# Performance work log

Hardware: AMD Instinct MI355X
Metric: run time of the kernel (lower is better)

The kernel has to match this reference:

```python
import jax, jax.numpy as jnp
import numpy as np

NUM_EXPERTS = 8
NUM_SLOTS = 4

def setup_inputs() -> dict:
    key = jax.random.key(0)
    k1, k2 = jax.random.split(key)
    B, S, D = 8, 4096, 1024
    x = jax.random.normal(k1, (B, S, D), dtype=jnp.float32)
    W_phi = jax.random.normal(k2, (D, NUM_EXPERTS * NUM_SLOTS), dtype=jnp.float32) * (1.0 / np.sqrt(D))
    b_phi = jnp.zeros((NUM_EXPERTS * NUM_SLOTS,), dtype=jnp.float32)
    return {"x": x, "W_phi": W_phi, "b_phi": b_phi}

def reference(x, W_phi, b_phi):
    B, S, D = x.shape
    E, P = NUM_EXPERTS, NUM_SLOTS
    # phi logits: (B, S, E, P)
    phi_logits = (jnp.einsum('bsd,dk->bsk', x, W_phi) + b_phi).reshape(B, S, E, P)
    # softmax over seq axis (dispatch weights)
    phi_weights = jax.nn.softmax(phi_logits, axis=1)
    # soft slots: weighted sum of tokens per (expert, slot) -> (B, E, P, D)
    # (faithful to expand_dims*multiply*sum-over-seq in the original, fused as einsum)
    soft_slots = jnp.einsum('bsep,bsd->bepd', phi_weights, x)
    expert_inputs = soft_slots.reshape(B, E, P * D)
    expert_weights = jnp.full((B, S, E), 1.0 / E, dtype=x.dtype)
    expert_indices = jnp.broadcast_to(jnp.arange(E, dtype=jnp.int32)[None, None, :], (B, S, E))
    raw_gate_probs = jax.nn.softmax(phi_logits, axis=-1)
    return (expert_weights, expert_indices, phi_weights, soft_slots, expert_inputs, phi_logits, raw_gate_probs)
```

## Files before the change

### kernel.cpp

```cpp
#include <hip/hip_runtime.h>
#include <hip/hip_bf16.h>

#define BB 8
#define SS 4096
#define DD 1024
#define KK 32
#define EE 8
#define PP 4

#define O0 0L
#define O1 262144L
#define O2 524288L
#define O3 1572864L
#define O4 1835008L
#define O5 2097152L
#define O6 3145728L

#define WA 0L
#define WB 8192L
#define WC 16384L
#define WPKH (WC + 2097152L)
#define WPKL (WPKH + 16384L)
#define WEND (WPKL + 16384L)

typedef __attribute__((ext_vector_type(8))) short short8v;
typedef __attribute__((ext_vector_type(4))) float f32x4;

__device__ __forceinline__ unsigned short f2bf(float f) {
    unsigned u = __builtin_bit_cast(unsigned, f);
    unsigned r = (u + 0x7FFFu + ((u >> 16) & 1u)) >> 16;
    return (unsigned short)r;
}
__device__ __forceinline__ float bf2f(unsigned short h) {
    return __builtin_bit_cast(float, (unsigned)h << 16);
}

__global__ __launch_bounds__(256) void k_wprep(const float* __restrict__ Wp,
    unsigned short* __restrict__ wh, unsigned short* __restrict__ wl)
{
    const int t  = blockIdx.x * 256 + threadIdx.x;
    const int l  = t & 63;
    const int tt = (t >> 6) & 1;
    const int ks = t >> 7;
    const int col = tt * 16 + (l & 15);
    const int dbase = ks * 32 + (l >> 4) * 8;
    const long obase = ((long)(ks * 2 + tt) * 64 + l) * 8;
#pragma unroll
    for (int j = 0; j < 8; ++j) {
        const float w = Wp[(long)(dbase + j) * KK + col];
        const unsigned short h = f2bf(w);
        const float lo = w - bf2f(h);
        wh[obase + j] = h;
        wl[obase + j] = f2bf(lo);
    }
}

__global__ __launch_bounds__(256) void k_logits_mfma(const float* __restrict__ x,
    const unsigned short* __restrict__ wh, const unsigned short* __restrict__ wl,
    float* __restrict__ wsP)
{
    const int tid  = threadIdx.x;
    const int wv   = tid >> 6;
    const int lane = tid & 63;
    const int blk  = blockIdx.x;
    const int tile = blk >> 1, half = blk & 1;
    const long tokw = (long)tile * 64 + wv * 16;
    const int mrow = lane & 15;
    const int kg   = lane >> 4;

    const float* xr = x + (tokw + mrow) * DD + half * 512 + kg * 8;
    const uint4* bh = reinterpret_cast<const uint4*>(wh) + (long)half * 16 * 2 * 64 + lane;
    const uint4* bl = reinterpret_cast<const uint4*>(wl) + (long)half * 16 * 2 * 64 + lane;

    f32x4 acc0 = {0.f, 0.f, 0.f, 0.f};
    f32x4 acc1 = {0.f, 0.f, 0.f, 0.f};

#pragma unroll 4
    for (int s = 0; s < 16; ++s) {
        const float4 u0 = *reinterpret_cast<const float4*>(xr + s * 32);
        const float4 u1 = *reinterpret_cast<const float4*>(xr + s * 32 + 4);
        const short8v b0h = __builtin_bit_cast(short8v, bh[(long)(s * 2    ) * 64]);
        const short8v b1h = __builtin_bit_cast(short8v, bh[(long)(s * 2 + 1) * 64]);
        const short8v b0l = __builtin_bit_cast(short8v, bl[(long)(s * 2    ) * 64]);
        const short8v b1l = __builtin_bit_cast(short8v, bl[(long)(s * 2 + 1) * 64]);

        const float xf[8] = {u0.x, u0.y, u0.z, u0.w, u1.x, u1.y, u1.z, u1.w};
        short8v ah, al;
#pragma unroll
        for (int j = 0; j < 8; ++j) {
            const unsigned u = __builtin_bit_cast(unsigned, xf[j]);
            ah[j] = (short)(u >> 16);
            const float hi = __builtin_bit_cast(float, u & 0xFFFF0000u);
            const float lo = xf[j] - hi;
            al[j] = (short)(__builtin_bit_cast(unsigned, lo) >> 16);
        }
        acc0 = __builtin_amdgcn_mfma_f32_16x16x32_bf16(ah, b0h, acc0, 0, 0, 0);
        acc1 = __builtin_amdgcn_mfma_f32_16x16x32_bf16(ah, b1h, acc1, 0, 0, 0);
        acc0 = __builtin_amdgcn_mfma_f32_16x16x32_bf16(al, b0h, acc0, 0, 0, 0);
        acc1 = __builtin_amdgcn_mfma_f32_16x16x32_bf16(al, b1h, acc1, 0, 0, 0);
        acc0 = __builtin_amdgcn_mfma_f32_16x16x32_bf16(ah, b0l, acc0, 0, 0, 0);
        acc1 = __builtin_amdgcn_mfma_f32_16x16x32_bf16(ah, b1l, acc1, 0, 0, 0);
    }

#pragma unroll
    for (int r = 0; r < 4; ++r) {
        const long tok = tokw + kg * 4 + r;
        float* o = wsP + ((long)half * 32768 + tok) * KK + mrow;
        o[0]  = acc0[r];
        o[16] = acc1[r];
    }
}

__global__ __launch_bounds__(256) void k_comb2(const float* __restrict__ wsP,
    const float* __restrict__ bp, float* __restrict__ out, float* __restrict__ ws)
{
    const int blk = blockIdx.x;
    const int tid = threadIdx.x;
    const int wv  = __builtin_amdgcn_readfirstlane(tid >> 6);
    const long g  = (long)blk * 256 + tid;
    float acc[KK];
#pragma unroll
    for (int k = 0; k < KK; ++k) acc[k] = bp[k];
#pragma unroll
    for (int h = 0; h < 2; ++h) {
        const float4* p = reinterpret_cast<const float4*>(wsP + ((long)h * 32768 + g) * KK);
#pragma unroll
        for (int m = 0; m < 8; ++m) {
            const float4 v = p[m];
            acc[4*m]   += v.x;
            acc[4*m+1] += v.y;
            acc[4*m+2] += v.z;
            acc[4*m+3] += v.w;
        }
    }
    float4* pl = reinterpret_cast<float4*>(out + O5 + g * KK);
#pragma unroll
    for (int m = 0; m < 8; ++m)
        pl[m] = make_float4(acc[4*m], acc[4*m+1], acc[4*m+2], acc[4*m+3]);
    float rg[KK];
#pragma unroll
    for (int e = 0; e < EE; ++e) {
        const float mx = fmaxf(fmaxf(acc[4*e], acc[4*e+1]), fmaxf(acc[4*e+2], acc[4*e+3]));
        float s = 0.f;
#pragma unroll
        for (int p = 0; p < PP; ++p) { rg[4*e+p] = __expf(acc[4*e+p] - mx); s += rg[4*e+p]; }
        const float ri = 1.f / s;
#pragma unroll
        for (int p = 0; p < PP; ++p) rg[4*e+p] *= ri;
    }
    float4* prg = reinterpret_cast<float4*>(out + O6 + g * KK);
#pragma unroll
    for (int m = 0; m < 8; ++m)
        prg[m] = make_float4(rg[4*m], rg[4*m+1], rg[4*m+2], rg[4*m+3]);
    float4* pew = reinterpret_cast<float4*>(out + O0 + g * EE);
    pew[0] = make_float4(0.125f, 0.125f, 0.125f, 0.125f);
    pew[1] = make_float4(0.125f, 0.125f, 0.125f, 0.125f);
    float4* pei = reinterpret_cast<float4*>(out + O1 + g * EE);
    pei[0] = make_float4(0.f, 1.f, 2.f, 3.f);
    pei[1] = make_float4(4.f, 5.f, 6.f, 7.f);

    float m[KK];
#pragma unroll
    for (int k = 0; k < KK; ++k) m[k] = acc[k];
    for (int off = 1; off < 64; off <<= 1) {
#pragma unroll
        for (int k = 0; k < KK; ++k) m[k] = fmaxf(m[k], __shfl_xor(m[k], off));
    }
    __shared__ float lm[4][KK];
    __shared__ float lsum[4][KK];
    if ((tid & 63) == 0) {
#pragma unroll
        for (int k = 0; k < KK; ++k) lm[wv][k] = m[k];
    }
    __syncthreads();
#pragma unroll
    for (int k = 0; k < KK; ++k)
        m[k] = fmaxf(fmaxf(lm[0][k], lm[1][k]), fmaxf(lm[2][k], lm[3][k]));
    float sv[KK];
#pragma unroll
    for (int k = 0; k < KK; ++k) sv[k] = __expf(acc[k] - m[k]);
    for (int off = 1; off < 64; off <<= 1) {
#pragma unroll
        for (int k = 0; k < KK; ++k) sv[k] += __shfl_xor(sv[k], off);
    }
    if ((tid & 63) == 0) {
#pragma unroll
        for (int k = 0; k < KK; ++k) lsum[wv][k] = sv[k];
    }
    __syncthreads();
    if (tid == 0) {
#pragma unroll
        for (int k = 0; k < KK; ++k) {
            ws[WA + (long)blk * 64 + k]      = m[k];
            ws[WA + (long)blk * 64 + 32 + k] = lsum[0][k] + lsum[1][k] + lsum[2][k] + lsum[3][k];
        }
    }
}

__global__ __launch_bounds__(256) void k_logits4(const float* __restrict__ x,
    const float* __restrict__ Wp, const float* __restrict__ bp,
    float* __restrict__ out)
{
    __shared__ float xl[2][64][68];
    __shared__ float wl[2][64][32];
    const int tid  = threadIdx.x;
    const int wv   = __builtin_amdgcn_readfirstlane(tid >> 6);
    const int lane = tid & 63;
    const long tok0 = (long)blockIdx.x * 64;
    const long g   = tok0 + lane;
    const int sr = tid >> 2;
    const int sco = (tid & 3) * 4;
    float acc[8];
#pragma unroll
    for (int j = 0; j < 8; ++j) acc[j] = 0.f;
    float4 xr[4], wr[2];
#pragma unroll
    for (int j = 0; j < 4; ++j)
        xr[j] = *reinterpret_cast<const float4*>(x + (tok0 + sr) * DD + sco + j * 16);
#pragma unroll
    for (int j = 0; j < 2; ++j)
        wr[j] = *reinterpret_cast<const float4*>(Wp + tid * 8 + j * 4);
#pragma unroll
    for (int j = 0; j < 4; ++j)
        *reinterpret_cast<float4*>(&xl[0][sr][sco + j * 16]) = xr[j];
#pragma unroll
    for (int j = 0; j < 2; ++j)
        *reinterpret_cast<float4*>(&wl[0][0][0] + tid * 8 + j * 4) = wr[j];
    __syncthreads();
    for (int c = 0; c < 16; ++c) {
        const int cb = c & 1;
        if (c < 15) {
            const long dg = (long)(c + 1) * 64;
#pragma unroll
            for (int j = 0; j < 4; ++j)
                xr[j] = *reinterpret_cast<const float4*>(
                    x + (tok0 + sr) * DD + dg + sco + j * 16);
#pragma unroll
            for (int j = 0; j < 2; ++j)
                wr[j] = *reinterpret_cast<const float4*>(Wp + dg * KK + tid * 8 + j * 4);
        }
        const float* xb = &xl[cb][lane][0];
        const float* wb = &wl[cb][0][0] + wv * 8;
#pragma unroll 4
        for (int dq = 0; dq < 16; ++dq) {
            const float4 xv = *reinterpret_cast<const float4*>(xb + dq * 4);
#pragma unroll
            for (int dd = 0; dd < 4; ++dd) {
                const float xs = (dd == 0) ? xv.x : (dd == 1) ? xv.y
                               : (dd == 2) ? xv.z : xv.w;
                const float4 w0 = *reinterpret_cast<const float4*>(wb + (dq * 4 + dd) * 32);
                const float4 w1 = *reinterpret_cast<const float4*>(wb + (dq * 4 + dd) * 32 + 4);
                acc[0] = fmaf(xs, w0.x, acc[0]);
                acc[1] = fmaf(xs, w0.y, acc[1]);
                acc[2] = fmaf(xs, w0.z, acc[2]);
                acc[3] = fmaf(xs, w0.w, acc[3]);
                acc[4] = fmaf(xs, w1.x, acc[4]);
                acc[5] = fmaf(xs, w1.y, acc[5]);
                acc[6] = fmaf(xs, w1.z, acc[6]);
                acc[7] = fmaf(xs, w1.w, acc[7]);
            }
        }
        if (c < 15) {
#pragma unroll
            for (int j = 0; j < 4; ++j)
                *reinterpret_cast<float4*>(&xl[cb ^ 1][sr][sco + j * 16]) = xr[j];
#pragma unroll
            for (int j = 0; j < 2; ++j)
                *reinterpret_cast<float4*>(&wl[cb ^ 1][0][0] + tid * 8 + j * 4) = wr[j];
        }
        __syncthreads();
    }
#pragma unroll
    for (int j = 0; j < 8; ++j) acc[j] += bp[wv * 8 + j];
    float* o5 = out + O5 + g * KK + wv * 8;
    *reinterpret_cast<float4*>(o5)     = make_float4(acc[0], acc[1], acc[2], acc[3]);
    *reinterpret_cast<float4*>(o5 + 4) = make_float4(acc[4], acc[5], acc[6], acc[7]);
    float rg[8];
#pragma unroll
    for (int e = 0; e < 2; ++e) {
        const float* aa = &acc[e * 4];
        const float m = fmaxf(fmaxf(aa[0], aa[1]), fmaxf(aa[2], aa[3]));
        float s = 0.f;
#pragma unroll
        for (int p = 0; p < PP; ++p) { rg[e*4+p] = __expf(aa[p] - m); s += rg[e*4+p]; }
        const float ri = 1.f / s;
#pragma unroll
        for (int p = 0; p < PP; ++p) rg[e*4+p] *= ri;
    }
    float* o6 = out + O6 + g * KK + wv * 8;
    *reinterpret_cast<float4*>(o6)     = make_float4(rg[0], rg[1], rg[2], rg[3]);
    *reinterpret_cast<float4*>(o6 + 4) = make_float4(rg[4], rg[5], rg[6], rg[7]);
    if (wv == 0) {
        float4* p = reinterpret_cast<float4*>(out + O0 + g * EE);
        p[0] = make_float4(0.125f, 0.125f, 0.125f, 0.125f);
        p[1] = make_float4(0.125f, 0.125f, 0.125f, 0.125f);
    } else if (wv == 1) {
        float4* p = reinterpret_cast<float4*>(out + O1 + g * EE);
        p[0] = make_float4(0.f, 1.f, 2.f, 3.f);
        p[1] = make_float4(4.f, 5.f, 6.f, 7.f);
    }
}

__global__ __launch_bounds__(256) void k_smpart(const float* __restrict__ out,
                                                float* __restrict__ ws)
{
    const int blk = blockIdx.x;
    const int tid = threadIdx.x;
    const int wv  = __builtin_amdgcn_readfirstlane(tid >> 6);
    const int b = blk >> 4, sc = blk & 15;
    const long s  = (long)sc * 256 + tid;
    const float* row = out + O5 + ((long)b * SS + s) * KK;
    float v[KK];
    const float4* r4 = reinterpret_cast<const float4*>(row);
#pragma unroll
    for (int q = 0; q < 8; ++q) {
        const float4 t = r4[q];
        v[4*q] = t.x; v[4*q+1] = t.y; v[4*q+2] = t.z; v[4*q+3] = t.w;
    }
    float m[KK];
#pragma unroll
    for (int k = 0; k < KK; ++k) m[k] = v[k];
    for (int off = 1; off < 64; off <<= 1) {
#pragma unroll
        for (int k = 0; k < KK; ++k) m[k] = fmaxf(m[k], __shfl_xor(m[k], off));
    }
    __shared__ float lm[4][KK];
    __shared__ float lsum[4][KK];
    if ((tid & 63) == 0) {
#pragma unroll
        for (int k = 0; k < KK; ++k) lm[wv][k] = m[k];
    }
    __syncthreads();
#pragma unroll
    for (int k = 0; k < KK; ++k)
        m[k] = fmaxf(fmaxf(lm[0][k], lm[1][k]), fmaxf(lm[2][k], lm[3][k]));
    float sv[KK];
#pragma unroll
    for (int k = 0; k < KK; ++k) sv[k] = __expf(v[k] - m[k]);
    for (int off = 1; off < 64; off <<= 1) {
#pragma unroll
        for (int k = 0; k < KK; ++k) sv[k] += __shfl_xor(sv[k], off);
    }
    if ((tid & 63) == 0) {
#pragma unroll
        for (int k = 0; k < KK; ++k) lsum[wv][k] = sv[k];
    }
    __syncthreads();
    if (tid == 0) {
#pragma unroll
        for (int k = 0; k < KK; ++k) {
            ws[WA + (long)blk * 64 + k]      = m[k];
            ws[WA + (long)blk * 64 + 32 + k] = lsum[0][k] + lsum[1][k] + lsum[2][k] + lsum[3][k];
        }
    }
}

__global__ __launch_bounds__(256) void k_pw2(float* __restrict__ out,
                                             const float* __restrict__ ws)
{
    __shared__ float sm[KK], srv[KK];
    const int tid = threadIdx.x;
    const long i4 = (long)blockIdx.x * 256 + tid;
    const long idx = i4 * 4;
    const int b = (int)(idx >> 17);
    if (tid < KK) {
        float m = -1e30f, s = 0.f;
        for (int c = 0; c < 16; ++c) {
            const float mc = ws[WA + (long)(b * 16 + c) * 64 + tid];
            const float sc = ws[WA + (long)(b * 16 + c) * 64 + 32 + tid];
            const float nm = fmaxf(m, mc);
            s = s * __expf(m - nm) + sc * __expf(mc - nm);
            m = nm;
        }
        sm[tid]  = m;
        srv[tid] = 1.f / s;
    }
    __syncthreads();
    const float4 l4 = reinterpret_cast<const float4*>(out + O5)[i4];
    const int k0 = (int)(idx & 31);
    const float r0 = __expf(l4.x - sm[k0])     * srv[k0];
    const float r1 = __expf(l4.y - sm[k0 + 1]) * srv[k0 + 1];
    const float r2 = __expf(l4.z - sm[k0 + 2]) * srv[k0 + 2];
    const float r3 = __expf(l4.w - sm[k0 + 3]) * srv[k0 + 3];
    reinterpret_cast<float4*>(out + O2)[i4] = make_float4(r0, r1, r2, r3);
}

__global__ __launch_bounds__(256) void k_slots4(const float* __restrict__ x,
    const float* __restrict__ out, float* __restrict__ dst, int SC, int SLEN)
{
    __shared__ float pwl[2][64 * KK];
    const int tid = threadIdx.x;
    const int blk = blockIdx.x;
    const int sc  = blk % SC;
    const int t2  = blk / SC;
    const int dc  = t2 & 1;
    const int b   = t2 >> 1;
    const int d   = dc * 512 + tid * 2;
    float2 acc[KK];
#pragma unroll
    for (int k = 0; k < KK; ++k) acc[k] = make_float2(0.f, 0.f);
    const long s0 = (long)sc * SLEN;
    const float* pw = out + O2 + ((long)b * SS + s0) * KK;
    const float* xp = x + ((long)b * SS + s0) * DD + d;
    const int NCH = SLEN >> 6;

    float4 r0 = *reinterpret_cast<const float4*>(pw + tid * 8);
    float4 r1 = *reinterpret_cast<const float4*>(pw + tid * 8 + 4);
    *reinterpret_cast<float4*>(&pwl[0][tid * 8])     = r0;
    *reinterpret_cast<float4*>(&pwl[0][tid * 8 + 4]) = r1;
    __syncthreads();

    for (int ch = 0; ch < NCH; ++ch) {
        const int cb = ch & 1;
        if (ch + 1 < NCH) {
            const float* pn = pw + (long)(ch + 1) * 64 * KK;
            r0 = *reinterpret_cast<const float4*>(pn + tid * 8);
            r1 = *reinterpret_cast<const float4*>(pn + tid * 8 + 4);
        }
        const float* xc = xp + (long)ch * 64 * DD;
        const float* pb = &pwl[cb][0];
#pragma unroll 4
        for (int i = 0; i < 64; ++i) {
            const float2 xv = *reinterpret_cast<const float2*>(xc + (long)i * DD);
#pragma unroll
            for (int q = 0; q < 8; ++q) {
                const float4 w = *reinterpret_cast<const float4*>(pb + i * KK + q * 4);
                acc[4*q].x   = fmaf(w.x, xv.x, acc[4*q].x);
                acc[4*q].y   = fmaf(w.x, xv.y, acc[4*q].y);
                acc[4*q+1].x = fmaf(w.y, xv.x, acc[4*q+1].x);
                acc[4*q+1].y = fmaf(w.y, xv.y, acc[4*q+1].y);
                acc[4*q+2].x = fmaf(w.z, xv.x, acc[4*q+2].x);
                acc[4*q+2].y = fmaf(w.z, xv.y, acc[4*q+2].y);
                acc[4*q+3].x = fmaf(w.w, xv.x, acc[4*q+3].x);
                acc[4*q+3].y = fmaf(w.w, xv.y, acc[4*q+3].y);
            }
        }
        if (ch + 1 < NCH) {
            *reinterpret_cast<float4*>(&pwl[cb ^ 1][tid * 8])     = r0;
            *reinterpret_cast<float4*>(&pwl[cb ^ 1][tid * 8 + 4]) = r1;
        }
        __syncthreads();
    }
    float* o = dst + ((long)(sc * BB + b) * KK) * DD + d;
#pragma unroll
    for (int k = 0; k < KK; ++k)
        *reinterpret_cast<float2*>(o + (long)k * DD) = acc[k];
}

__global__ __launch_bounds__(256) void k_red(const float* __restrict__ src,
                                             float* __restrict__ out, int SC)
{
    const long i4 = (long)blockIdx.x * 256 + threadIdx.x;
    float4 s = make_float4(0.f, 0.f, 0.f, 0.f);
    const float4* p = reinterpret_cast<const float4*>(src);
    for (int c = 0; c < SC; ++c) {
        const float4 t = p[(long)c * 65536 + i4];
        s.x += t.x; s.y += t.y; s.z += t.z; s.w += t.w;
    }
    reinterpret_cast<float4*>(out + O3)[i4] = s;
    reinterpret_cast<float4*>(out + O4)[i4] = s;
}

extern "C" void kernel_launch(void* const* d_in, const int* in_sizes, int n_in,
                              void* d_out, int out_size, void* d_ws, size_t ws_size,
                              hipStream_t stream)
{
    const float* x  = (const float*)d_in[0];
    const float* Wp = (const float*)d_in[1];
    const float* bp = (const float*)d_in[2];
    float* out = (float*)d_out;
    float* ws  = (float*)d_ws;

    const size_t wfloats = ws_size / 4;

    if (wfloats >= (size_t)WEND) {
        unsigned short* wh = (unsigned short*)(ws + WPKH);
        unsigned short* wl = (unsigned short*)(ws + WPKL);
        hipLaunchKernelGGL(k_wprep,       dim3(16),   dim3(256), 0, stream, Wp, wh, wl);
        hipLaunchKernelGGL(k_logits_mfma, dim3(1024), dim3(256), 0, stream, x, wh, wl, ws + WC);
        hipLaunchKernelGGL(k_comb2,       dim3(128),  dim3(256), 0, stream, ws + WC, bp, out, ws);
    } else {
        hipLaunchKernelGGL(k_logits4, dim3(512), dim3(256), 0, stream, x, Wp, bp, out);
        hipLaunchKernelGGL(k_smpart,  dim3(128), dim3(256), 0, stream, out, ws);
    }

    hipLaunchKernelGGL(k_pw2, dim3(1024), dim3(256), 0, stream, out, ws);

    int SC = 0;
    if      (wfloats >= (size_t)(WC + 32L * 262144)) SC = 32;
    else if (wfloats >= (size_t)(WC + 16L * 262144)) SC = 16;
    else if (wfloats >= (size_t)(WC +  8L * 262144)) SC = 8;
    else if (wfloats >= (size_t)(WC +  4L * 262144)) SC = 4;
    else if (wfloats >= (size_t)(WC +  2L * 262144)) SC = 2;
    else if (wfloats >= (size_t)(WC +  1L * 262144)) SC = 1;

    if (SC >= 1) {
        hipLaunchKernelGGL(k_slots4, dim3(BB * 2 * SC), dim3(256), 0, stream,
                           x, out, ws + WC, SC, SS / SC);
        hipLaunchKernelGGL(k_red,    dim3(256), dim3(256), 0, stream, ws + WC, out, SC);
    } else {
        hipLaunchKernelGGL(k_slots4, dim3(BB * 2), dim3(256), 0, stream,
                           x, out, out + O3, 1, SS);
        hipLaunchKernelGGL(k_red,    dim3(256), dim3(256), 0, stream, out + O3, out, 1);
    }
}
```

Baseline: 108.7 us.

## Fuse logits combine into MFMA kernel and retile slot accumulation

The MFMA logits kernel now covers the full D per block, so it no longer writes two partial halves to workspace. It transposes its results through shared memory and does the bias add, expert softmax, constant outputs and per-block seq max/sum in the same kernel, which removes the separate combine kernel and its workspace round trip. The seq-softmax partials grow to 64 chunks per batch, so k_pw2 takes the chunk count as a parameter. The slot-sum kernel switches from two columns per thread to one, with four d-chunks per batch and at most 16 seq splits, trading fewer registers for more blocks and less reuse of each pw value loaded from shared memory.

```diff
diff --git a/kernel.cpp b/kernel.cpp
--- a/kernel.cpp
+++ b/kernel.cpp
@@ -17,11 +17,10 @@
 #define O6 3145728L
 
 #define WA 0L
-#define WB 8192L
-#define WC 16384L
-#define WPKH (WC + 2097152L)
-#define WPKL (WPKH + 16384L)
-#define WEND (WPKL + 16384L)
+#define WB 32768L
+#define WPKH 33280L
+#define WPKL 49664L
+#define WC 66048L
 
 typedef __attribute__((ext_vector_type(8))) short short8v;
 typedef __attribute__((ext_vector_type(4))) float f32x4;
@@ -55,28 +54,31 @@
     }
 }
 
-__global__ __launch_bounds__(256) void k_logits_mfma(const float* __restrict__ x,
+__global__ __launch_bounds__(256) void k_logits_f(const float* __restrict__ x,
     const unsigned short* __restrict__ wh, const unsigned short* __restrict__ wl,
-    float* __restrict__ wsP)
-{
+    const float* __restrict__ bp, float* __restrict__ out, float* __restrict__ ws)
+{
+    __shared__ float sT[64][33];
+    __shared__ float lm[4][KK];
+    __shared__ float lsum[4][KK];
     const int tid  = threadIdx.x;
     const int wv   = tid >> 6;
     const int lane = tid & 63;
     const int blk  = blockIdx.x;
-    const int tile = blk >> 1, half = blk & 1;
-    const long tokw = (long)tile * 64 + wv * 16;
+    const long tok0 = (long)blk * 64;
+    const long tokw = tok0 + wv * 16;
     const int mrow = lane & 15;
     const int kg   = lane >> 4;
 
-    const float* xr = x + (tokw + mrow) * DD + half * 512 + kg * 8;
-    const uint4* bh = reinterpret_cast<const uint4*>(wh) + (long)half * 16 * 2 * 64 + lane;
-    const uint4* bl = reinterpret_cast<const uint4*>(wl) + (long)half * 16 * 2 * 64 + lane;
+    const float* xr = x + (tokw + mrow) * DD + kg * 8;
+    const uint4* bh = reinterpret_cast<const uint4*>(wh) + lane;
+    const uint4* bl = reinterpret_cast<const uint4*>(wl) + lane;
 
     f32x4 acc0 = {0.f, 0.f, 0.f, 0.f};
     f32x4 acc1 = {0.f, 0.f, 0.f, 0.f};
 
 #pragma unroll 4
-    for (int s = 0; s < 16; ++s) {
+    for (int s = 0; s < 32; ++s) {
         const float4 u0 = *reinterpret_cast<const float4*>(xr + s * 32);
         const float4 u1 = *reinterpret_cast<const float4*>(xr + s * 32 + 4);
         const short8v b0h = __builtin_bit_cast(short8v, bh[(long)(s * 2    ) * 64]);
@@ -104,96 +106,78 @@
 
 #pragma unroll
     for (int r = 0; r < 4; ++r) {
-        const long tok = tokw + kg * 4 + r;
-        float* o = wsP + ((long)half * 32768 + tok) * KK + mrow;
-        o[0]  = acc0[r];
-        o[16] = acc1[r];
-    }
-}
-
-__global__ __launch_bounds__(256) void k_comb2(const float* __restrict__ wsP,
-    const float* __restrict__ bp, float* __restrict__ out, float* __restrict__ ws)
-{
-    const int blk = blockIdx.x;
-    const int tid = threadIdx.x;
-    const int wv  = __builtin_amdgcn_readfirstlane(tid >> 6);
-    const long g  = (long)blk * 256 + tid;
-    float acc[KK];
-#pragma unroll
-    for (int k = 0; k < KK; ++k) acc[k] = bp[k];
-#pragma unroll
-    for (int h = 0; h < 2; ++h) {
-        const float4* p = reinterpret_cast<const float4*>(wsP + ((long)h * 32768 + g) * KK);
-#pragma unroll
-        for (int m = 0; m < 8; ++m) {
-            const float4 v = p[m];
-            acc[4*m]   += v.x;
-            acc[4*m+1] += v.y;
-            acc[4*m+2] += v.z;
-            acc[4*m+3] += v.w;
-        }
-    }
-    float4* pl = reinterpret_cast<float4*>(out + O5 + g * KK);
-#pragma unroll
-    for (int m = 0; m < 8; ++m)
-        pl[m] = make_float4(acc[4*m], acc[4*m+1], acc[4*m+2], acc[4*m+3]);
-    float rg[KK];
-#pragma unroll
-    for (int e = 0; e < EE; ++e) {
-        const float mx = fmaxf(fmaxf(acc[4*e], acc[4*e+1]), fmaxf(acc[4*e+2], acc[4*e+3]));
+        sT[wv * 16 + kg * 4 + r][mrow]      = acc0[r];
+        sT[wv * 16 + kg * 4 + r][16 + mrow] = acc1[r];
+    }
+    __syncthreads();
+
+    const int tl = tid >> 2;
+    const int kq = tid & 3;
+    float a[8];
+#pragma unroll
+    for (int j = 0; j < 8; ++j) a[j] = sT[tl][kq * 8 + j] + bp[kq * 8 + j];
+    const long g = tok0 + tl;
+    float* o5 = out + O5 + g * KK + kq * 8;
+    *reinterpret_cast<float4*>(o5)     = make_float4(a[0], a[1], a[2], a[3]);
+    *reinterpret_cast<float4*>(o5 + 4) = make_float4(a[4], a[5], a[6], a[7]);
+    float rg[8];
+#pragma unroll
+    for (int e = 0; e < 2; ++e) {
+        const float* aa = &a[e * 4];
+        const float mx = fmaxf(fmaxf(aa[0], aa[1]), fmaxf(aa[2], aa[3]));
         float s = 0.f;
 #pragma unroll
-        for (int p = 0; p < PP; ++p) { rg[4*e+p] = __expf(acc[4*e+p] - mx); s += rg[4*e+p]; }
+        for (int p = 0; p < PP; ++p) { rg[e*4+p] = __expf(aa[p] - mx); s += rg[e*4+p]; }
         const float ri = 1.f / s;
 #pragma unroll
-        for (int p = 0; p < PP; ++p) rg[4*e+p] *= ri;
-    }
-    float4* prg = reinterpret_cast<float4*>(out + O6 + g * KK);
-#pragma unroll
-    for (int m = 0; m < 8; ++m)
-        prg[m] = make_float4(rg[4*m], rg[4*m+1], rg[4*m+2], rg[4*m+3]);
-    float4* pew = reinterpret_cast<float4*>(out + O0 + g * EE);
-    pew[0] = make_float4(0.125f, 0.125f, 0.125f, 0.125f);
-    pew[1] = make_float4(0.125f, 0.125f, 0.125f, 0.125f);
-    float4* pei = reinterpret_cast<float4*>(out + O1 + g * EE);
-    pei[0] = make_float4(0.f, 1.f, 2.f, 3.f);
-    pei[1] = make_float4(4.f, 5.f, 6.f, 7.f);
-
-    float m[KK];
-#pragma unroll
-    for (int k = 0; k < KK; ++k) m[k] = acc[k];
-    for (int off = 1; off < 64; off <<= 1) {
-#pragma unroll
-        for (int k = 0; k < KK; ++k) m[k] = fmaxf(m[k], __shfl_xor(m[k], off));
-    }
-    __shared__ float lm[4][KK];
-    __shared__ float lsum[4][KK];
-    if ((tid & 63) == 0) {
-#pragma unroll
-        for (int k = 0; k < KK; ++k) lm[wv][k] = m[k];
-    }
-    __syncthreads();
-#pragma unroll
-    for (int k = 0; k < KK; ++k)
-        m[k] = fmaxf(fmaxf(lm[0][k], lm[1][k]), fmaxf(lm[2][k], lm[3][k]));
-    float sv[KK];
-#pragma unroll
-    for (int k = 0; k < KK; ++k) sv[k] = __expf(acc[k] - m[k]);
-    for (int off = 1; off < 64; off <<= 1) {
-#pragma unroll
-        for (int k = 0; k < KK; ++k) sv[k] += __shfl_xor(sv[k], off);
-    }
-    if ((tid & 63) == 0) {
-#pragma unroll
-        for (int k = 0; k < KK; ++k) lsum[wv][k] = sv[k];
-    }
-    __syncthreads();
-    if (tid == 0) {
-#pragma unroll
-        for (int k = 0; k < KK; ++k) {
-            ws[WA + (long)blk * 64 + k]      = m[k];
-            ws[WA + (long)blk * 64 + 32 + k] = lsum[0][k] + lsum[1][k] + lsum[2][k] + lsum[3][k];
-        }
+        for (int p = 0; p < PP; ++p) rg[e*4+p] *= ri;
+    }
+    float* o6 = out + O6 + g * KK + kq * 8;
+    *reinterpret_cast<float4*>(o6)     = make_float4(rg[0], rg[1], rg[2], rg[3]);
+    *reinterpret_cast<float4*>(o6 + 4) = make_float4(rg[4], rg[5], rg[6], rg[7]);
+    if (tid < 128) {
+        const int t = tid >> 1, h = tid & 1;
+        reinterpret_cast<float4*>(out + O0 + (tok0 + t) * EE)[h] =
+            make_float4(0.125f, 0.125f, 0.125f, 0.125f);
+        reinterpret_cast<float4*>(out + O1 + (tok0 + t) * EE)[h] =
+            h ? make_float4(4.f, 5.f, 6.f, 7.f) : make_float4(0.f, 1.f, 2.f, 3.f);
+    }
+
+    float mv[8];
+#pragma unroll
+    for (int j = 0; j < 8; ++j) mv[j] = a[j];
+    for (int mask = 4; mask < 64; mask <<= 1) {
+#pragma unroll
+        for (int j = 0; j < 8; ++j) mv[j] = fmaxf(mv[j], __shfl_xor(mv[j], mask));
+    }
+    if (lane < 4) {
+#pragma unroll
+        for (int j = 0; j < 8; ++j) lm[wv][lane * 8 + j] = mv[j];
+    }
+    __syncthreads();
+    float mfin[8];
+#pragma unroll
+    for (int j = 0; j < 8; ++j) {
+        const int k = kq * 8 + j;
+        mfin[j] = fmaxf(fmaxf(lm[0][k], lm[1][k]), fmaxf(lm[2][k], lm[3][k]));
+    }
+    float sv[8];
+#pragma unroll
+    for (int j = 0; j < 8; ++j) sv[j] = __expf(a[j] - mfin[j]);
+    for (int mask = 4; mask < 64; mask <<= 1) {
+#pragma unroll
+        for (int j = 0; j < 8; ++j) sv[j] += __shfl_xor(sv[j], mask);
+    }
+    if (lane < 4) {
+#pragma unroll
+        for (int j = 0; j < 8; ++j) lsum[wv][lane * 8 + j] = sv[j];
+    }
+    __syncthreads();
+    if (tid < KK) {
+        ws[WA + (long)blk * 64 + tid] =
+            fmaxf(fmaxf(lm[0][tid], lm[1][tid]), fmaxf(lm[2][tid], lm[3][tid]));
+        ws[WA + (long)blk * 64 + 32 + tid] =
+            lsum[0][tid] + lsum[1][tid] + lsum[2][tid] + lsum[3][tid];
     }
 }
 
@@ -356,7 +340,7 @@
 }
 
 __global__ __launch_bounds__(256) void k_pw2(float* __restrict__ out,
-                                             const float* __restrict__ ws)
+                                             const float* __restrict__ ws, int CPB)
 {
     __shared__ float sm[KK], srv[KK];
     const int tid = threadIdx.x;
@@ -365,9 +349,9 @@
     const int b = (int)(idx >> 17);
     if (tid < KK) {
         float m = -1e30f, s = 0.f;
-        for (int c = 0; c < 16; ++c) {
-            const float mc = ws[WA + (long)(b * 16 + c) * 64 + tid];
-            const float sc = ws[WA + (long)(b * 16 + c) * 64 + 32 + tid];
+        for (int c = 0; c < CPB; ++c) {
+            const float mc = ws[WA + (long)(b * CPB + c) * 64 + tid];
+            const float sc = ws[WA + (long)(b * CPB + c) * 64 + 32 + tid];
             const float nm = fmaxf(m, mc);
             s = s * __expf(m - nm) + sc * __expf(mc - nm);
             m = nm;
@@ -385,7 +369,7 @@
     reinterpret_cast<float4*>(out + O2)[i4] = make_float4(r0, r1, r2, r3);
 }
 
-__global__ __launch_bounds__(256) void k_slots4(const float* __restrict__ x,
+__global__ __launch_bounds__(256) void k_slots2(const float* __restrict__ x,
     const float* __restrict__ out, float* __restrict__ dst, int SC, int SLEN)
 {
     __shared__ float pwl[2][64 * KK];
@@ -393,12 +377,12 @@
     const int blk = blockIdx.x;
     const int sc  = blk % SC;
     const int t2  = blk / SC;
-    const int dc  = t2 & 1;
-    const int b   = t2 >> 1;
-    const int d   = dc * 512 + tid * 2;
-    float2 acc[KK];
-#pragma unroll
-    for (int k = 0; k < KK; ++k) acc[k] = make_float2(0.f, 0.f);
+    const int dc  = t2 & 3;
+    const int b   = t2 >> 2;
+    const int d   = dc * 256 + tid;
+    float acc[KK];
+#pragma unroll
+    for (int k = 0; k < KK; ++k) acc[k] = 0.f;
     const long s0 = (long)sc * SLEN;
     const float* pw = out + O2 + ((long)b * SS + s0) * KK;
     const float* xp = x + ((long)b * SS + s0) * DD + d;
@@ -419,20 +403,16 @@
         }
         const float* xc = xp + (long)ch * 64 * DD;
         const float* pb = &pwl[cb][0];
-#pragma unroll 4
+#pragma unroll 8
         for (int i = 0; i < 64; ++i) {
-            const float2 xv = *reinterpret_cast<const float2*>(xc + (long)i * DD);
+            const float xv = xc[(long)i * DD];
 #pragma unroll
             for (int q = 0; q < 8; ++q) {
                 const float4 w = *reinterpret_cast<const float4*>(pb + i * KK + q * 4);
-                acc[4*q].x   = fmaf(w.x, xv.x, acc[4*q].x);
-                acc[4*q].y   = fmaf(w.x, xv.y, acc[4*q].y);
-                acc[4*q+1].x = fmaf(w.y, xv.x, acc[4*q+1].x);
-                acc[4*q+1].y = fmaf(w.y, xv.y, acc[4*q+1].y);
-                acc[4*q+2].x = fmaf(w.z, xv.x, acc[4*q+2].x);
-                acc[4*q+2].y = fmaf(w.z, xv.y, acc[4*q+2].y);
-                acc[4*q+3].x = fmaf(w.w, xv.x, acc[4*q+3].x);
-                acc[4*q+3].y = fmaf(w.w, xv.y, acc[4*q+3].y);
+                acc[4*q]   = fmaf(w.x, xv, acc[4*q]);
+                acc[4*q+1] = fmaf(w.y, xv, acc[4*q+1]);
+                acc[4*q+2] = fmaf(w.z, xv, acc[4*q+2]);
+                acc[4*q+3] = fmaf(w.w, xv, acc[4*q+3]);
             }
         }
         if (ch + 1 < NCH) {
@@ -443,8 +423,7 @@
     }
     float* o = dst + ((long)(sc * BB + b) * KK) * DD + d;
 #pragma unroll
-    for (int k = 0; k < KK; ++k)
-        *reinterpret_cast<float2*>(o + (long)k * DD) = acc[k];
+    for (int k = 0; k < KK; ++k) o[(long)k * DD] = acc[k];
 }
 
 __global__ __launch_bounds__(256) void k_red(const float* __restrict__ src,
@@ -472,34 +451,36 @@
     float* ws  = (float*)d_ws;
 
     const size_t wfloats = ws_size / 4;
-
-    if (wfloats >= (size_t)WEND) {
+    const bool mfma_ok = wfloats >= (size_t)WC;
+    int CPB;
+
+    if (mfma_ok) {
         unsigned short* wh = (unsigned short*)(ws + WPKH);
         unsigned short* wl = (unsigned short*)(ws + WPKL);
-        hipLaunchKernelGGL(k_wprep,       dim3(16),   dim3(256), 0, stream, Wp, wh, wl);
-        hipLaunchKernelGGL(k_logits_mfma, dim3(1024), dim3(256), 0, stream, x, wh, wl, ws + WC);
-        hipLaunchKernelGGL(k_comb2,       dim3(128),  dim3(256), 0, stream, ws + WC, bp, out, ws);
+        hipLaunchKernelGGL(k_wprep,    dim3(16),  dim3(256), 0, stream, Wp, wh, wl);
+        hipLaunchKernelGGL(k_logits_f, dim3(512), dim3(256), 0, stream, x, wh, wl, bp, out, ws);
+        CPB = 64;
     } else {
         hipLaunchKernelGGL(k_logits4, dim3(512), dim3(256), 0, stream, x, Wp, bp, out);
         hipLaunchKernelGGL(k_smpart,  dim3(128), dim3(256), 0, stream, out, ws);
-    }
-
-    hipLaunchKernelGGL(k_pw2, dim3(1024), dim3(256), 0, stream, out, ws);
+        CPB = 16;
+    }
+
+    hipLaunchKernelGGL(k_pw2, dim3(1024), dim3(256), 0, stream, out, ws, CPB);
 
     int SC = 0;
-    if      (wfloats >= (size_t)(WC + 32L * 262144)) SC = 32;
-    else if (wfloats >= (size_t)(WC + 16L * 262144)) SC = 16;
+    if      (wfloats >= (size_t)(WC + 16L * 262144)) SC = 16;
     else if (wfloats >= (size_t)(WC +  8L * 262144)) SC = 8;
     else if (wfloats >= (size_t)(WC +  4L * 262144)) SC = 4;
     else if (wfloats >= (size_t)(WC +  2L * 262144)) SC = 2;
     else if (wfloats >= (size_t)(WC +  1L * 262144)) SC = 1;
 
     if (SC >= 1) {
-        hipLaunchKernelGGL(k_slots4, dim3(BB * 2 * SC), dim3(256), 0, stream,
+        hipLaunchKernelGGL(k_slots2, dim3(BB * 4 * SC), dim3(256), 0, stream,
                            x, out, ws + WC, SC, SS / SC);
         hipLaunchKernelGGL(k_red,    dim3(256), dim3(256), 0, stream, ws + WC, out, SC);
     } else {
-        hipLaunchKernelGGL(k_slots4, dim3(BB * 2), dim3(256), 0, stream,
+        hipLaunchKernelGGL(k_slots2, dim3(BB * 4), dim3(256), 0, stream,
                            x, out, out + O3, 1, SS);
         hipLaunchKernelGGL(k_red,    dim3(256), dim3(256), 0, stream, out + O3, out, 1);
     }
```

Result: slower. 114.9 us (+5.7%).
